# Kernel tuning notes

Hardware: AMD Instinct MI355X
Metric: run time of the kernel (lower is better)

The kernel has to match this reference:

```python
import jax, jax.numpy as jnp
from jax import lax
import numpy as np

N_NODES = 8192
N_FEATURES = 1024
N_FILTRATIONS = 4
HIDDEN_DIM = 64
MAX_DEG = 8            # fixed out-degree used when generating edge_list
N_EDGES = N_NODES * MAX_DEG


def setup_inputs() -> dict:
    key = jax.random.key(0)
    ks = jax.random.split(key, 10)
    X = jax.random.normal(ks[0], (N_NODES, N_FEATURES), dtype=jnp.float32)
    # directed edge list, exactly MAX_DEG out-edges per node
    src = jnp.repeat(jnp.arange(N_NODES, dtype=jnp.int32), MAX_DEG)
    dst = jax.random.randint(ks[1], (N_EDGES,), 0, N_NODES, dtype=jnp.int32)
    edge_list = jnp.stack([src, dst], axis=0)
    # filtrations_nn: Linear(n_features,32) -> ReLU -> Linear(32,n_filtrations)
    W1 = jax.random.normal(ks[2], (32, N_FEATURES), dtype=jnp.float32) * 0.05
    b1 = jnp.zeros((32,), jnp.float32)
    W2 = jax.random.normal(ks[3], (N_FILTRATIONS, 32), dtype=jnp.float32) * 0.05
    b2 = jnp.zeros((N_FILTRATIONS,), jnp.float32)
    # deep sets: theta = Linear(2*n_filtrations, hidden), rho = Linear(1, n_features)
    Wt = jax.random.normal(ks[4], (HIDDEN_DIM, 2 * N_FILTRATIONS), dtype=jnp.float32) * 0.05
    bt = jnp.zeros((HIDDEN_DIM,), jnp.float32)
    Wr = jax.random.normal(ks[5], (N_FEATURES, 1), dtype=jnp.float32) * 0.05
    br = jnp.zeros((N_FEATURES,), jnp.float32)
    return {"X": X, "edge_list": edge_list, "W1": W1, "b1": b1, "W2": W2,
            "b2": b2, "Wt": Wt, "bt": bt, "Wr": Wr, "br": br}


def uf_find(parent, node):
    # chase parent pointers until a root (parent[v] == v)
    return lax.while_loop(lambda v: parent[v] != v, lambda v: parent[v], node)


def build_neighbor_table(edge_list, n_nodes, max_deg):
    # padded CSR-style neighbor table (n_nodes, max_deg), -1 = no edge
    src = edge_list[0].astype(jnp.int32)
    dst = edge_list[1].astype(jnp.int32)
    e = src.shape[0]
    order_e = jnp.argsort(src)  # stable
    src_s, dst_s = src[order_e], dst[order_e]
    counts = jnp.zeros(n_nodes, jnp.int32).at[src].add(1)
    offsets = jnp.concatenate([jnp.zeros(1, jnp.int32), jnp.cumsum(counts)[:-1].astype(jnp.int32)])
    slot = jnp.arange(e, dtype=jnp.int32) - offsets[src_s]
    return jnp.full((n_nodes, max_deg), -1, jnp.int32).at[src_s, slot].set(dst_s)


def persistence_dim0(values, nbr_table):
    """0-dim persistence via sequential union-find with elder rule.
    Row for sort-position j: (birth=j, death=step when the component born at j is absorbed).
    Returned indexed by node id (diagram[order[j]] = row j), matching the torch code."""
    n = values.shape[0]
    order = jnp.argsort(values).astype(jnp.int32)  # filtration order
    pos = jnp.zeros(n, jnp.int32).at[order].set(jnp.arange(n, dtype=jnp.int32))  # rank
    parent0 = jnp.arange(n, dtype=jnp.int32)
    deaths0 = jnp.zeros(n, jnp.float32)

    def step_fn(carry, sv):
        parent, deaths = carry
        s, vertex = sv
        nbrs = nbr_table[vertex]

        def edge_body(k, pc):
            parent, deaths = pc
            u = nbrs[k]
            u_c = jnp.maximum(u, 0)
            valid = (u >= 0) & (pos[u_c] <= s)  # neighbor already activated
            u_eff = jnp.where(valid, u_c, vertex)
            r1 = uf_find(parent, vertex)
            r2 = uf_find(parent, u_eff)
            parent = parent.at[vertex].set(r1).at[u_eff].set(r2)  # path compression
            merge = r1 != r2
            older_is_r1 = pos[r1] < pos[r2]
            absorbed = jnp.where(older_is_r1, r2, r1)   # younger root dies (elder rule)
            survivor = jnp.where(older_is_r1, r1, r2)
            parent = parent.at[absorbed].set(jnp.where(merge, survivor, absorbed))
            dp = pos[absorbed]
            deaths = deaths.at[dp].set(jnp.where(merge, s.astype(jnp.float32), deaths[dp]))
            return (parent, deaths)

        parent, deaths = lax.fori_loop(0, MAX_DEG, edge_body, (parent, deaths))
        return (parent, deaths), None

    (_, deaths), _ = lax.scan(step_fn, (parent0, deaths0),
                              (jnp.arange(n, dtype=jnp.int32), order))
    # finalize: undying components -> inf in the original; use finite cap n for numerics
    deaths = jnp.where(deaths == 0.0, jnp.float32(n), deaths)
    births = jnp.arange(n, dtype=jnp.float32)
    diag_sorted = jnp.stack([births, deaths], axis=1)  # (n, 2), row j = sort position j
    return jnp.zeros((n, 2), jnp.float32).at[order].set(diag_sorted)


def reference(X, edge_list, W1, b1, W2, b2, Wt, bt, Wr, br):
    n = X.shape[0]
    # filtrations_nn
    h = jax.nn.relu(X @ W1.T + b1)
    filt = h @ W2.T + b2                      # (n, n_filtrations)
    filt_ng = lax.stop_gradient(filt)         # diagram is piecewise constant in filt
    nbr_table = build_neighbor_table(edge_list, n, MAX_DEG)
    pds = [persistence_dim0(filt_ng[:, i], nbr_table) for i in range(N_FILTRATIONS)]
    pd = jnp.stack(pds, axis=0).transpose(1, 0, 2).reshape(n, 2 * N_FILTRATIONS)
    # DeepSetsAggregation(theta, rho) with index=zeros(hidden_dim), dim=1:
    theta = pd @ Wt.T + bt                    # (n, hidden)
    pooled = jnp.sum(theta, axis=1, keepdims=True)  # segment-sum of dim 1 into one bucket
    x_hat = pooled @ Wr.T + br                # (n, n_features)
    return X + x_hat
```

## Files before the change

### kernel.cpp

```cpp
#include <hip/hip_runtime.h>

#define N_NODES     8192
#define N_FEAT      1024
#define N_FILT      4
#define MAXDEG      8
#define BLK         256

__global__ __launch_bounds__(256) void filt_kernel(
    const float* __restrict__ X, const float* __restrict__ W1,
    const float* __restrict__ b1, const float* __restrict__ W2,
    const float* __restrict__ b2, float* __restrict__ filtT)
{
    const int node = blockIdx.x * 8 + (threadIdx.x >> 5);
    const int h    = threadIdx.x & 31;
    const float* xr = X  + (size_t)node * N_FEAT;
    const float* wr = W1 + (size_t)h    * N_FEAT;
    float acc = 0.f;
    for (int j = 0; j < N_FEAT; j += 4) {
        float4 xv = *reinterpret_cast<const float4*>(xr + j);
        float4 wv = *reinterpret_cast<const float4*>(wr + j);
        acc += xv.x * wv.x + xv.y * wv.y + xv.z * wv.z + xv.w * wv.w;
    }
    float hv = fmaxf(acc + b1[h], 0.f);
    #pragma unroll
    for (int fo = 0; fo < N_FILT; ++fo) {
        float v = hv * W2[fo * 32 + h];
        for (int off = 16; off; off >>= 1) v += __shfl_xor(v, off, 32);
        if (h == 0) filtT[fo * N_NODES + node] = v + b2[fo];
    }
}

__global__ void wsum_kernel(const float* __restrict__ Wt,
                            const float* __restrict__ bt,
                            float* __restrict__ wsum)
{
    int t = threadIdx.x;
    if (t < 8) {
        float s = 0.f;
        for (int hh = 0; hh < 64; ++hh) s += Wt[hh * 8 + t];
        wsum[t] = s;
    } else if (t == 8) {
        float s = 0.f;
        for (int hh = 0; hh < 64; ++hh) s += bt[hh];
        wsum[8] = s;
    }
}

__global__ __launch_bounds__(256) void rank_partial_kernel(
    const float* __restrict__ filtT, unsigned short* __restrict__ partial)
{
    const int b  = blockIdx.x;
    const int f  = b >> 7;
    const int cs = (b >> 5) & 3;
    const int cv = b & 31;
    const int v  = (cv << 8) + threadIdx.x;
    const float myv = filtT[(f << 13) + v];

    __shared__ float4 tile[512];
    const float4* src = reinterpret_cast<const float4*>(filtT + (f << 13) + cs * 2048);
    for (int i = threadIdx.x; i < 512; i += 256) tile[i] = src[i];
    __syncthreads();

    int cnt = 0;
    const int ubase = cs * 2048;
    #pragma unroll 4
    for (int j = 0; j < 512; ++j) {
        float4 wv = tile[j];
        int u = ubase + j * 4;
        cnt += (wv.x < myv) || (wv.x == myv && (u + 0) < v);
        cnt += (wv.y < myv) || (wv.y == myv && (u + 1) < v);
        cnt += (wv.z < myv) || (wv.z == myv && (u + 2) < v);
        cnt += (wv.w < myv) || (wv.w == myv && (u + 3) < v);
    }
    partial[((f * 4 + cs) << 13) + v] = (unsigned short)cnt;
}

__global__ __launch_bounds__(256) void rank_final_kernel(
    const unsigned short* __restrict__ partial,
    unsigned short* __restrict__ pos16, unsigned short* __restrict__ order16)
{
    int g = blockIdx.x * 256 + threadIdx.x;
    int f = g >> 13, v = g & 8191;
    int r = (int)partial[((f * 4 + 0) << 13) + v]
          + (int)partial[((f * 4 + 1) << 13) + v]
          + (int)partial[((f * 4 + 2) << 13) + v]
          + (int)partial[((f * 4 + 3) << 13) + v];
    pos16[(f << 13) + v] = (unsigned short)r;
    order16[(f << 13) + r] = (unsigned short)v;
}

__global__ __launch_bounds__(256) void etable_kernel(
    const unsigned short* __restrict__ order16,
    const unsigned short* __restrict__ pos16,
    const int* __restrict__ edge_dst,
    unsigned short* __restrict__ et)
{
    const int f  = blockIdx.x >> 5;
    const int e0 = ((blockIdx.x & 31) << 11);
    for (int i = threadIdx.x; i < 2048; i += 256) {
        int e = e0 + i;
        int s = e >> 3, k = e & 7;
        int v = (int)order16[(f << 13) + s];
        int u = edge_dst[v * MAXDEG + k];
        int q = (int)pos16[(f << 13) + u];
        et[(size_t)f * (N_NODES * MAXDEG) + e] = (unsigned short)(q < s ? q : s);
    }
}

__device__ __forceinline__ int row8min(int v) {
    int t = min(v, __builtin_amdgcn_mov_dpp(v, 0xB1, 0xF, 0xF, true));
    t = min(t, __builtin_amdgcn_mov_dpp(t, 0x4E, 0xF, 0xF, true));
    t = min(t, __builtin_amdgcn_mov_dpp(t, 0x141, 0xF, 0xF, true));
    return t;
}

__global__ __launch_bounds__(256) void persist_kernel(
    const unsigned short* __restrict__ et,
    const unsigned short* __restrict__ pos16,
    unsigned short* __restrict__ death16)
{
    const int f    = blockIdx.x;
    const int tid  = threadIdx.x;
    const int lane = tid & 63;
    const int w    = tid >> 6;

    __shared__ unsigned int   s_pd[N_NODES];
    __shared__ unsigned short s_r16[BLK][8];
    __shared__ unsigned short s_list[BLK];
    __shared__ int s_wc[4];
    volatile unsigned int* vpd = s_pd;

    for (int v = tid; v < N_NODES; v += 256) s_pd[v] = (unsigned)v;
    __syncthreads();

    const unsigned short* etf = et + (size_t)f * (N_NODES * MAXDEG);

    for (int lo = 0; lo < N_NODES; lo += BLK) {
        const int s = lo + tid;

        uint4 raw = *reinterpret_cast<const uint4*>(etf + (size_t)s * 8);
        int e8[8];
        e8[0] = raw.x & 0xffff; e8[1] = raw.x >> 16;
        e8[2] = raw.y & 0xffff; e8[3] = raw.y >> 16;
        e8[4] = raw.z & 0xffff; e8[5] = raw.z >> 16;
        e8[6] = raw.w & 0xffff; e8[7] = raw.w >> 16;

        int pk[8];
        #pragma unroll
        for (int k = 0; k < 8; ++k) pk[k] = e8[k];
        for (;;) {
            int qk[8];
            #pragma unroll
            for (int k = 0; k < 8; ++k) qk[k] = (int)(vpd[pk[k]] & 0xffffu);
            bool done = true;
            #pragma unroll
            for (int k = 0; k < 8; ++k) { done &= (qk[k] == pk[k]); pk[k] = qk[k]; }
            if (done) break;
        }
        int first = -1; bool same = true;
        #pragma unroll
        for (int k = 0; k < 8; ++k) {
            if (e8[k] == s) continue;
            if (first < 0) first = pk[k];
            else same &= (pk[k] == first);
        }
        bool cand = (first >= 0) && !same;
        if (first >= 0 && same)
            vpd[s] = (unsigned)first | ((unsigned)s << 16);

        __syncthreads();

        bool impure = false;
        if (cand) {
            for (;;) {
                int qk[8];
                #pragma unroll
                for (int k = 0; k < 8; ++k) qk[k] = (int)(vpd[pk[k]] & 0xffffu);
                bool done = true;
                #pragma unroll
                for (int k = 0; k < 8; ++k) { done &= (qk[k] == pk[k]); pk[k] = qk[k]; }
                if (done) break;
            }
            int f2 = -1; bool same2 = true;
            #pragma unroll
            for (int k = 0; k < 8; ++k) {
                if (e8[k] == s) continue;
                if (f2 < 0) f2 = pk[k];
                else same2 &= (pk[k] == f2);
            }
            if (same2) {
                vpd[s] = (unsigned)f2 | ((unsigned)s << 16);
            } else {
                impure = true;
                #pragma unroll
                for (int k = 0; k < 8; ++k) s_r16[tid][k] = (unsigned short)pk[k];
            }
        }

        unsigned long long bal = __ballot(impure);
        int within = __popcll(bal & ((1ull << lane) - 1ull));
        if (lane == 0) s_wc[w] = __popcll(bal);
        __syncthreads();
        int base = 0, total = 0;
        #pragma unroll
        for (int i = 0; i < 4; ++i) { int c = s_wc[i]; if (i < w) base += c; total += c; }
        if (impure) s_list[base + within] = (unsigned short)tid;
        __syncthreads();

        if (tid < 64 && total > 0) {
            int t_cur = (int)s_list[0];
            int p_cur = (int)s_r16[t_cur][lane & 7];
            for (int i = 0; i < total; ++i) {
                int t_nxt = (int)s_list[(i + 1 < total) ? (i + 1) : i];
                int p_nxt = (int)s_r16[t_nxt][lane & 7];
                const int sv = lo + t_cur;
                int p = p_cur;
                for (;;) {
                    int q = (int)(vpd[p] & 0xffffu);
                    if (__all(q == p)) break;
                    p = q;
                }
                int m = row8min(p);
                if (lane < 8 && p != m)
                    vpd[p] = (unsigned)m | ((unsigned)sv << 16);
                if (lane == 0)
                    vpd[sv] = (unsigned)m | ((unsigned)sv << 16);
                t_cur = t_nxt; p_cur = p_nxt;
            }
        }
        __syncthreads();
    }

    for (int n = tid; n < N_NODES; n += 256) {
        int p = (int)pos16[(f << 13) + n];
        int d = (int)(s_pd[p] >> 16);
        death16[(f << 13) + n] = (unsigned short)(d ? d : N_NODES);
    }
}

__global__ __launch_bounds__(256) void out_kernel(
    const float* __restrict__ X, const float* __restrict__ Wr,
    const float* __restrict__ br,
    const unsigned short* __restrict__ pos16,
    const unsigned short* __restrict__ death16,
    const float* __restrict__ wsum,
    float* __restrict__ out)
{
    const int node = blockIdx.x;
    float pl = wsum[8];
    #pragma unroll
    for (int i = 0; i < N_FILT; ++i) {
        pl += (float)pos16[(i << 13) + node]   * wsum[2 * i + 0]
            + (float)death16[(i << 13) + node] * wsum[2 * i + 1];
    }
    const int fb = threadIdx.x * 4;
    const float4 xv = *reinterpret_cast<const float4*>(X + (size_t)node * N_FEAT + fb);
    const float4 wv = *reinterpret_cast<const float4*>(Wr + fb);
    const float4 bv = *reinterpret_cast<const float4*>(br + fb);
    float4 o;
    o.x = xv.x + pl * wv.x + bv.x;
    o.y = xv.y + pl * wv.y + bv.y;
    o.z = xv.z + pl * wv.z + bv.z;
    o.w = xv.w + pl * wv.w + bv.w;
    *reinterpret_cast<float4*>(out + (size_t)node * N_FEAT + fb) = o;
}

extern "C" void kernel_launch(void* const* d_in, const int* in_sizes, int n_in,
                              void* d_out, int out_size, void* d_ws, size_t ws_size,
                              hipStream_t stream) {
    const float* X  = (const float*)d_in[0];
    const int* edge = (const int*)d_in[1];
    const float* W1 = (const float*)d_in[2];
    const float* b1 = (const float*)d_in[3];
    const float* W2 = (const float*)d_in[4];
    const float* b2 = (const float*)d_in[5];
    const float* Wt = (const float*)d_in[6];
    const float* bt = (const float*)d_in[7];
    const float* Wr = (const float*)d_in[8];
    const float* br = (const float*)d_in[9];

    const int* edge_dst = edge + N_NODES * MAXDEG;

    char* wsb = (char*)d_ws;
    float*          filtT   = (float*)(wsb);
    unsigned short* pos16   = (unsigned short*)(wsb + 131072);
    unsigned short* order16 = (unsigned short*)(wsb + 196608);
    unsigned short* death16 = (unsigned short*)(wsb + 196608);
    unsigned short* partial = (unsigned short*)(wsb + 262144);
    unsigned short* et      = (unsigned short*)(wsb + 262144);
    float*          wsum    = (float*)(wsb + 786432);

    hipLaunchKernelGGL(filt_kernel,  dim3(N_NODES / 8), dim3(256), 0, stream,
                       X, W1, b1, W2, b2, filtT);
    hipLaunchKernelGGL(wsum_kernel,  dim3(1), dim3(64), 0, stream, Wt, bt, wsum);
    hipLaunchKernelGGL(rank_partial_kernel, dim3(512), dim3(256), 0, stream,
                       filtT, partial);
    hipLaunchKernelGGL(rank_final_kernel, dim3(128), dim3(256), 0, stream,
                       partial, pos16, order16);
    hipLaunchKernelGGL(etable_kernel, dim3(4 * 32), dim3(256), 0, stream,
                       order16, pos16, edge_dst, et);
    hipLaunchKernelGGL(persist_kernel, dim3(N_FILT), dim3(256), 0, stream,
                       et, pos16, death16);
    hipLaunchKernelGGL(out_kernel,   dim3(N_NODES), dim3(256), 0, stream,
                       X, Wr, br, pos16, death16, wsum, (float*)d_out);
}
```

Baseline: 640.3 us.

## Add extra parallel resolution round and process eight impure nodes per wave step

The per-block union-find for 0-dim persistence gets a third parallel resolution phase. Candidates that remain ambiguous write a provisional min-root parent, which leaves fewer nodes for the serial single-wave pass. The serial pass now handles eight impure nodes per iteration across the 64 lanes, one 8-lane group per node. Later groups apply the earlier groups' merges by forwarding through readlane, so the serial merge order is kept. The pointer chase also skips lanes whose root is already resolved. This adds synchronisation rounds and a complex forwarding loop that could be subtly incorrect.

```diff
diff --git a/kernel.cpp b/kernel.cpp
--- a/kernel.cpp
+++ b/kernel.cpp
@@ -114,6 +114,22 @@
     return t;
 }
 
+__device__ __forceinline__ void chase8m(volatile unsigned int* vpd, int (&pk)[8]) {
+    unsigned msk = 0;
+    for (;;) {
+        bool all = true;
+        #pragma unroll
+        for (int k = 0; k < 8; ++k) {
+            if (!(msk & (1u << k))) {
+                int q = (int)(vpd[pk[k]] & 0xffffu);
+                if (q == pk[k]) msk |= (1u << k);
+                else { pk[k] = q; all = false; }
+            }
+        }
+        if (all) break;
+    }
+}
+
 __global__ __launch_bounds__(256) void persist_kernel(
     const unsigned short* __restrict__ et,
     const unsigned short* __restrict__ pos16,
@@ -126,6 +142,7 @@
 
     __shared__ unsigned int   s_pd[N_NODES];
     __shared__ unsigned short s_r16[BLK][8];
+    __shared__ unsigned char  s_flag[BLK];
     __shared__ unsigned short s_list[BLK];
     __shared__ int s_wc[4];
     volatile unsigned int* vpd = s_pd;
@@ -144,59 +161,70 @@
         e8[2] = raw.y & 0xffff; e8[3] = raw.y >> 16;
         e8[4] = raw.z & 0xffff; e8[5] = raw.z >> 16;
         e8[6] = raw.w & 0xffff; e8[7] = raw.w >> 16;
-
         int pk[8];
         #pragma unroll
         for (int k = 0; k < 8; ++k) pk[k] = e8[k];
-        for (;;) {
-            int qk[8];
-            #pragma unroll
-            for (int k = 0; k < 8; ++k) qk[k] = (int)(vpd[pk[k]] & 0xffffu);
-            bool done = true;
-            #pragma unroll
-            for (int k = 0; k < 8; ++k) { done &= (qk[k] == pk[k]); pk[k] = qk[k]; }
-            if (done) break;
-        }
-        int first = -1; bool same = true;
-        #pragma unroll
-        for (int k = 0; k < 8; ++k) {
-            if (e8[k] == s) continue;
-            if (first < 0) first = pk[k];
-            else same &= (pk[k] == first);
-        }
-        bool cand = (first >= 0) && !same;
-        if (first >= 0 && same)
-            vpd[s] = (unsigned)first | ((unsigned)s << 16);
-
-        __syncthreads();
-
-        bool impure = false;
-        if (cand) {
-            for (;;) {
-                int qk[8];
-                #pragma unroll
-                for (int k = 0; k < 8; ++k) qk[k] = (int)(vpd[pk[k]] & 0xffffu);
-                bool done = true;
-                #pragma unroll
-                for (int k = 0; k < 8; ++k) { done &= (qk[k] == pk[k]); pk[k] = qk[k]; }
-                if (done) break;
-            }
-            int f2 = -1; bool same2 = true;
+        chase8m(vpd, pk);
+        {
+            int first = -1; bool same = true;
             #pragma unroll
             for (int k = 0; k < 8; ++k) {
-                if (e8[k] == s) continue;
-                if (f2 < 0) f2 = pk[k];
-                else same2 &= (pk[k] == f2);
-            }
-            if (same2) {
-                vpd[s] = (unsigned)f2 | ((unsigned)s << 16);
-            } else {
+                if (pk[k] == s) continue;
+                if (first < 0) first = pk[k];
+                else same &= (pk[k] == first);
+            }
+            bool cand = (first >= 0) && !same;
+            if (first >= 0 && same)
+                vpd[s] = (unsigned)first | ((unsigned)s << 16);
+            if (cand) {
+                #pragma unroll
+                for (int k = 0; k < 8; ++k) s_r16[tid][k] = (unsigned short)pk[k];
+            }
+            s_flag[tid] = cand ? 2 : 0;
+        }
+        __syncthreads();
+
+        {
+            bool cand2 = false;
+            if (s_flag[tid] == 2) {
+                #pragma unroll
+                for (int k = 0; k < 8; ++k) pk[k] = (int)s_r16[tid][k];
+                chase8m(vpd, pk);
+                int first = -1; bool same = true; int m = pk[0];
+                #pragma unroll
+                for (int k = 0; k < 8; ++k) {
+                    m = min(m, pk[k]);
+                    if (pk[k] == s) continue;
+                    if (first < 0) first = pk[k];
+                    else same &= (pk[k] == first);
+                }
+                if (same) {
+                    vpd[s] = (unsigned)first | ((unsigned)s << 16);
+                } else {
+                    cand2 = true;
+                    vpd[s] = (unsigned)m | ((unsigned)s << 16);
+                    #pragma unroll
+                    for (int k = 0; k < 8; ++k) s_r16[tid][k] = (unsigned short)pk[k];
+                }
+            }
+            s_flag[tid] = cand2 ? 2 : 0;
+        }
+        __syncthreads();
+
+        bool impure = false;
+        if (s_flag[tid] == 2) {
+            #pragma unroll
+            for (int k = 0; k < 8; ++k) pk[k] = (int)s_r16[tid][k];
+            chase8m(vpd, pk);
+            bool same = true;
+            #pragma unroll
+            for (int k = 1; k < 8; ++k) same &= (pk[k] == pk[0]);
+            if (!same) {
                 impure = true;
                 #pragma unroll
                 for (int k = 0; k < 8; ++k) s_r16[tid][k] = (unsigned short)pk[k];
             }
         }
-
         unsigned long long bal = __ballot(impure);
         int within = __popcll(bal & ((1ull << lane) - 1ull));
         if (lane == 0) s_wc[w] = __popcll(bal);
@@ -207,25 +235,46 @@
         if (impure) s_list[base + within] = (unsigned short)tid;
         __syncthreads();
 
-        if (tid < 64 && total > 0) {
-            int t_cur = (int)s_list[0];
-            int p_cur = (int)s_r16[t_cur][lane & 7];
-            for (int i = 0; i < total; ++i) {
-                int t_nxt = (int)s_list[(i + 1 < total) ? (i + 1) : i];
-                int p_nxt = (int)s_r16[t_nxt][lane & 7];
-                const int sv = lo + t_cur;
-                int p = p_cur;
+        if (w == 0 && total > 0) {
+            const int g    = lane >> 3;
+            const int slot = lane & 7;
+            int idx0 = g; if (idx0 >= total) idx0 = total - 1;
+            int t_n = (int)s_list[idx0];
+            int p_n = (int)s_r16[t_n][slot];
+            for (int bs = 0; bs < total; bs += 8) {
+                const int t = t_n;
+                int p = p_n;
+                const int sv = lo + t;
+                const int nb = bs + 8;
+                if (nb < total) {
+                    int ni = nb + g; if (ni >= total) ni = total - 1;
+                    t_n = (int)s_list[ni];
+                    p_n = (int)s_r16[t_n][slot];
+                }
                 for (;;) {
                     int q = (int)(vpd[p] & 0xffffu);
-                    if (__all(q == p)) break;
+                    if (q == p) break;
                     p = q;
                 }
-                int m = row8min(p);
-                if (lane < 8 && p != m)
-                    vpd[p] = (unsigned)m | ((unsigned)sv << 16);
-                if (lane == 0)
-                    vpd[sv] = (unsigned)m | ((unsigned)sv << 16);
-                t_cur = t_nxt; p_cur = p_nxt;
+                int pack = 0;
+                #pragma unroll
+                for (int gg = 0; gg < 8; ++gg) {
+                    if (gg > 0) {
+                        #pragma unroll
+                        for (int k = 0; k < 8; ++k) {
+                            int o = __builtin_amdgcn_readlane(pack, (gg - 1) * 8 + k);
+                            if ((o & (1 << 26)) && p == (o & 0x1fff))
+                                p = (o >> 13) & 0x1fff;
+                        }
+                    }
+                    int m = row8min(p);
+                    if (g == gg) {
+                        bool kill = (p != m);
+                        pack = p | (m << 13) | (kill ? (1 << 26) : 0);
+                        if (kill)
+                            vpd[p] = (unsigned)m | ((unsigned)sv << 16);
+                    }
+                }
             }
         }
         __syncthreads();
```

After: 870.5 us. 1.36x slower.
